# Performance work log

Hardware: AMD Instinct MI355X
Metric: run time of the kernel (lower is better)

The kernel has to match this reference:

```python
import jax, jax.numpy as jnp
import numpy as np

K = 3   # up_kernel
S = 2   # scale_factor per stage
COMP = 64  # compressed channels (mmcv CARAFEPack default)


def _conv2d(x, w, b, pad):
    y = jax.lax.conv_general_dilated(
        x, w, window_strides=(1, 1), padding=[(pad, pad), (pad, pad)],
        dimension_numbers=('NCHW', 'OIHW', 'NCHW'))
    return y + b[None, :, None, None]


def _carafe_stage(x, wc, bc, we, be):
    B, C, H, W = x.shape
    # kernel prediction branch
    comp = _conv2d(x, wc, bc, 0)                 # [B, 64, H, W]
    m = _conv2d(comp, we, be, 1)                 # [B, K*K*S*S, H, W]
    # pixel shuffle: [B, K*K, S, S, H, W] -> [B, K*K, H, S, W, S]
    m = m.reshape(B, K * K, S, S, H, W).transpose(0, 1, 4, 2, 5, 3)
    # softmax over the K*K kernel weights per output pixel
    m = jax.nn.softmax(m, axis=1)                # [B, 9, H, S, W, S]
    # 3x3 neighborhoods of source (row-major kernel order, matching mmcv)
    xp = jnp.pad(x, ((0, 0), (0, 0), (1, 1), (1, 1)))
    patches = jnp.stack(
        [xp[:, :, dy:dy + H, dx:dx + W] for dy in range(K) for dx in range(K)],
        axis=2)                                   # [B, C, 9, H, W]
    # content-aware reassembly: weights shared across channels (up_group=1)
    out = jnp.einsum('bckhw,bkhpwq->bchpwq', patches, m)
    return out.reshape(B, C, S * H, S * W)


def setup_inputs() -> dict:
    key = jax.random.key(0)
    ks = jax.random.split(key, 12)
    B, C, H, W = 2, 256, 16, 16
    inp = {
        'source': jax.random.normal(ks[0], (B, C, H, W), jnp.float32),
        'guidance': jax.random.normal(ks[1], (B, 3, 256, 256), jnp.float32),
    }
    sc = 1.0 / np.sqrt(C)        # fan-in of 1x1 compressor
    se = 1.0 / np.sqrt(COMP * K * K)  # fan-in of 3x3 encoder
    for i in range(4):
        inp[f'wc{i+1}'] = jax.random.normal(ks[2 + 2 * i], (COMP, C, 1, 1), jnp.float32) * sc
        inp[f'bc{i+1}'] = jnp.zeros((COMP,), jnp.float32)
        inp[f'we{i+1}'] = jax.random.normal(ks[3 + 2 * i], (K * K * S * S, COMP, K, K), jnp.float32) * se
        inp[f'be{i+1}'] = jnp.zeros((K * K * S * S,), jnp.float32)
    return inp


def reference(source, guidance,
              wc1, bc1, we1, be1,
              wc2, bc2, we2, be2,
              wc3, bc3, we3, be3,
              wc4, bc4, we4, be4):
    x = _carafe_stage(source, wc1, bc1, we1, be1)
    x = _carafe_stage(x, wc2, bc2, we2, be2)
    x = _carafe_stage(x, wc3, bc3, we3, be3)
    x = _carafe_stage(x, wc4, bc4, we4, be4)
    return x
```

## Files before the change

kernel.cpp:

```cpp
#include <hip/hip_runtime.h>

#define LB __launch_bounds__(256)

__global__ LB void prep_weights(
    const float* __restrict__ wcA, const float* __restrict__ wcB,
    const float* __restrict__ wcC, const float* __restrict__ wcD,
    const float* __restrict__ weA, const float* __restrict__ weB,
    const float* __restrict__ weC, const float* __restrict__ weD,
    float* __restrict__ wcT, float* __restrict__ weT, float* __restrict__ weT3)
{
    int seg = blockIdx.y;
    int t = blockIdx.x * 256 + threadIdx.x;
    if (seg < 4) {
        if (t >= 64 * 256) return;
        const float* w = (seg == 0) ? wcA : (seg == 1) ? wcB : (seg == 2) ? wcC : wcD;
        int c = t & 255, o = t >> 8;
        wcT[seg * 16384 + c * 64 + o] = w[t];
    } else if (seg < 8) {
        if (t >= 36 * 64 * 9) return;
        const float* w = (seg == 4) ? weA : (seg == 5) ? weB : (seg == 6) ? weC : weD;
        int kt = t % 9;
        int r = t / 9;
        int i = r & 63;
        int o = r >> 6;
        int kk = o >> 2, pq = o & 3;
        weT[(seg - 4) * 36864 + ((pq * 64 + i) * 9 + kt) * 16 + kk] = w[t];
    } else {
        if (t >= 36 * 64 * 9) return;
        const float* w = (seg == 8) ? weA : (seg == 9) ? weB : (seg == 10) ? weC : weD;
        int kt = t % 9;
        int r = t / 9;
        int i = r & 63;
        int o = r >> 6;
        weT3[(seg - 8) * 23040 + (i * 9 + kt) * 40 + o] = w[t];
    }
}

template<int OPT>
__global__ LB void compress_flat_k(const float* __restrict__ x, const float* __restrict__ wcO,
                                   const float* __restrict__ bc, float* __restrict__ comp,
                                   int lgW, int lgNpix)
{
    const int lgHW = 2 * lgW;
    const int HW = 1 << lgHW;
    int tid = blockIdx.x * 256 + threadIdx.x;
    int px = tid & ((1 << lgNpix) - 1);
    int og = __builtin_amdgcn_readfirstlane(tid >> lgNpix);
    int b = px >> lgHW;
    int hw = px & (HW - 1);
    const float* xp = x + (((size_t)b * 256) << lgHW) + hw;

    float acc[OPT];
    #pragma unroll
    for (int j = 0; j < OPT; j++) acc[j] = bc[og * OPT + j];

    for (int c0 = 0; c0 < 256; c0 += 8) {
        float xv[8];
        #pragma unroll
        for (int u = 0; u < 8; u++) xv[u] = xp[(size_t)(c0 + u) << lgHW];
        #pragma unroll
        for (int j = 0; j < OPT; j++) {
            const float* wr = wcO + (og * OPT + j) * 256 + c0;
            #pragma unroll
            for (int u = 0; u < 8; u++) acc[j] += wr[u] * xv[u];
        }
    }
    float* op = comp + (((size_t)b * 64 + og * OPT) << lgHW) + hw;
    #pragma unroll
    for (int j = 0; j < OPT; j++) op[(size_t)j << lgHW] = acc[j];
}

__global__ LB void compress_k(const float* __restrict__ x, const float* __restrict__ wcT,
                              const float* __restrict__ bc, float* __restrict__ comp, int lgW)
{
    const int lgHW = 2 * lgW;
    const int HW = 1 << lgHW;
    int lane = threadIdx.x & 63;
    int og = __builtin_amdgcn_readfirstlane(threadIdx.x >> 6);
    int pix = blockIdx.x * 64 + lane;
    int b = pix >> lgHW;
    int hw = pix & (HW - 1);
    const float* xp = x + (((size_t)b * 256) << lgHW) + hw;
    const float* wr = wcT + og * 16;

    float acc[16];
    #pragma unroll
    for (int j = 0; j < 16; j++) acc[j] = bc[og * 16 + j];

    for (int c0 = 0; c0 < 256; c0 += 16) {
        float xv[16];
        #pragma unroll
        for (int u = 0; u < 16; u++)
            xv[u] = xp[(size_t)(c0 + u) << lgHW];
        #pragma unroll
        for (int u = 0; u < 16; u++) {
            const float* w = wr + (c0 + u) * 64;
            float4 w0 = *(const float4*)(w);
            float4 w1 = *(const float4*)(w + 4);
            float4 w2 = *(const float4*)(w + 8);
            float4 w3 = *(const float4*)(w + 12);
            float xu = xv[u];
            acc[0]  += w0.x * xu; acc[1]  += w0.y * xu; acc[2]  += w0.z * xu; acc[3]  += w0.w * xu;
            acc[4]  += w1.x * xu; acc[5]  += w1.y * xu; acc[6]  += w1.z * xu; acc[7]  += w1.w * xu;
            acc[8]  += w2.x * xu; acc[9]  += w2.y * xu; acc[10] += w2.z * xu; acc[11] += w2.w * xu;
            acc[12] += w3.x * xu; acc[13] += w3.y * xu; acc[14] += w3.z * xu; acc[15] += w3.w * xu;
        }
    }

    float* op = comp + (((size_t)b * 64 + og * 16) << lgHW) + hw;
    #pragma unroll
    for (int j = 0; j < 16; j++) op[(size_t)j << lgHW] = acc[j];
}

__global__ LB void encoder_wave_k(const float* __restrict__ comp, const float* __restrict__ weT3,
                                  const float* __restrict__ be, float* __restrict__ mnorm, int lgW)
{
    const int lgHW = 2 * lgW;
    const int HW = 1 << lgHW, W = 1 << lgW, H = W;
    int lane = threadIdx.x & 63;
    int wid = threadIdx.x >> 6;
    int pix = blockIdx.x * 4 + wid;
    int b = pix >> lgHW;
    int hw = pix & (HW - 1);
    int h = hw >> lgW, w = hw & (W - 1);
    int o = lane < 36 ? lane : 35;

    int off[9];
    float msk[9];
    #pragma unroll
    for (int ky = 0; ky < 3; ky++) {
        int ys = h + ky - 1;
        bool yok = (unsigned)ys < (unsigned)H;
        #pragma unroll
        for (int kx = 0; kx < 3; kx++) {
            int xs = w + kx - 1;
            bool ok = yok && ((unsigned)xs < (unsigned)W);
            int kt = ky * 3 + kx;
            off[kt] = ok ? ((ys << lgW) + xs) : 0;
            msk[kt] = ok ? 1.f : 0.f;
        }
    }

    float acc = be[o];
    const float* cb = comp + (((size_t)b) << lgHW) * 64;
    for (int c = 0; c < 64; c += 2) {
        const float* ci0 = cb + ((size_t)c << lgHW);
        const float* ci1 = cb + ((size_t)(c + 1) << lgHW);
        float tap[2][9];
        #pragma unroll
        for (int kt = 0; kt < 9; kt++) tap[0][kt] = ci0[off[kt]];
        #pragma unroll
        for (int kt = 0; kt < 9; kt++) tap[1][kt] = ci1[off[kt]];
        const float* wr0 = weT3 + (c * 9) * 40 + o;
        #pragma unroll
        for (int u = 0; u < 2; u++) {
            #pragma unroll
            for (int kt = 0; kt < 9; kt++)
                acc += wr0[(u * 9 + kt) * 40] * (tap[u][kt] * msk[kt]);
        }
    }

    int pq = o & 3;
    float m = acc;
    #pragma unroll
    for (int j = 0; j < 9; j++) m = fmaxf(m, __shfl(acc, pq + j * 4, 64));
    float e = __expf(acc - m);
    float ssum = 0.f;
    #pragma unroll
    for (int j = 0; j < 9; j++) ssum += __shfl(e, pq + j * 4, 64);
    if (lane < 36)
        mnorm[((((size_t)b * 36) + o) << lgHW) + hw] = e / ssum;
}

__global__ LB void encoder_k(const float* __restrict__ comp, const float* __restrict__ weT,
                             const float* __restrict__ be, float* __restrict__ mnorm, int lgW)
{
    const int lgHW = 2 * lgW;
    const int HW = 1 << lgHW, W = 1 << lgW, H = W;
    int lane = threadIdx.x & 63;
    int pq = __builtin_amdgcn_readfirstlane(threadIdx.x >> 6);
    int pix = blockIdx.x * 64 + lane;
    int b = pix >> lgHW;
    int hw = pix & (HW - 1);
    int h = hw >> lgW, w = hw & (W - 1);

    int off[9];
    float msk[9];
    #pragma unroll
    for (int ky = 0; ky < 3; ky++) {
        int ys = h + ky - 1;
        bool yok = (unsigned)ys < (unsigned)H;
        #pragma unroll
        for (int kx = 0; kx < 3; kx++) {
            int xs = w + kx - 1;
            bool ok = yok && ((unsigned)xs < (unsigned)W);
            int kt = ky * 3 + kx;
            off[kt] = ok ? ((ys << lgW) + xs) : 0;
            msk[kt] = ok ? 1.f : 0.f;
        }
    }

    float acc[9];
    #pragma unroll
    for (int kk = 0; kk < 9; kk++) acc[kk] = be[kk * 4 + pq];

    const float* wp = weT + pq * 9216;
    const float* cb = comp + (((size_t)b) << lgHW) * 64;
    for (int i = 0; i < 64; i += 2) {
        const float* ci0 = cb + ((size_t)i << lgHW);
        const float* ci1 = cb + ((size_t)(i + 1) << lgHW);
        float tap[2][9];
        #pragma unroll
        for (int kt = 0; kt < 9; kt++) tap[0][kt] = ci0[off[kt]];
        #pragma unroll
        for (int kt = 0; kt < 9; kt++) tap[1][kt] = ci1[off[kt]];
        #pragma unroll
        for (int u = 0; u < 2; u++) {
            const float* wi = wp + (i + u) * 144;
            #pragma unroll
            for (int kt = 0; kt < 9; kt++) {
                const float* wt = wi + kt * 16;
                float4 w0 = *(const float4*)(wt);
                float4 w1 = *(const float4*)(wt + 4);
                float  w8 = wt[8];
                float tv = tap[u][kt] * msk[kt];
                acc[0] += w0.x * tv; acc[1] += w0.y * tv; acc[2] += w0.z * tv;
                acc[3] += w0.w * tv; acc[4] += w1.x * tv; acc[5] += w1.y * tv;
                acc[6] += w1.z * tv; acc[7] += w1.w * tv; acc[8] += w8 * tv;
            }
        }
    }

    float m = acc[0];
    #pragma unroll
    for (int kk = 1; kk < 9; kk++) m = fmaxf(m, acc[kk]);
    float s = 0.f;
    #pragma unroll
    for (int kk = 0; kk < 9; kk++) { acc[kk] = __expf(acc[kk] - m); s += acc[kk]; }
    float r = 1.f / s;
    float* mp = mnorm + (((size_t)b * 36) << lgHW) + hw;
    #pragma unroll
    for (int kk = 0; kk < 9; kk++) mp[(size_t)(kk * 4 + pq) << lgHW] = acc[kk] * r;
}

template<int CPT>
__global__ LB void reassembly_k(const float* __restrict__ x, const float* __restrict__ mnorm,
                                float* __restrict__ out, int lgW)
{
    const int lgHW = 2 * lgW;
    const int HW = 1 << lgHW, W = 1 << lgW, H = W;
    int lane = threadIdx.x & 63;
    int cg = threadIdx.x >> 6;
    int nbsh = lgHW - 5;
    int pb = blockIdx.x & ((1 << nbsh) - 1);
    int cs = blockIdx.x >> nbsh;
    int pix = pb * 64 + lane;
    int b = pix >> lgHW;
    int hw = pix & (HW - 1);
    int h = hw >> lgW, w = hw & (W - 1);

    int off[9];
    float msk[9];
    #pragma unroll
    for (int ky = 0; ky < 3; ky++) {
        int ys = h + ky - 1;
        bool yok = (unsigned)ys < (unsigned)H;
        #pragma unroll
        for (int kx = 0; kx < 3; kx++) {
            int xs = w + kx - 1;
            bool ok = yok && ((unsigned)xs < (unsigned)W);
            int kt = ky * 3 + kx;
            off[kt] = ok ? ((ys << lgW) + xs) : 0;
            msk[kt] = ok ? 1.f : 0.f;
        }
    }
    const float* mp = mnorm + (((size_t)b * 36) << lgHW) + hw;
    float wreg[36];
    #pragma unroll
    for (int ch = 0; ch < 36; ch++) wreg[ch] = mp[(size_t)ch << lgHW];

    int c0 = (cs * 4 + cg) * CPT;
    const float* xb = x + ((size_t)b * 256 + c0) * HW;
    size_t OW = (size_t)W * 2;
    float* ob = out + (((size_t)b * 256 + c0) * 2 * H + 2 * h) * OW + 2 * w;
    for (int it = 0; it < CPT; it += 2) {
        const float* xc0 = xb + ((size_t)it << lgHW);
        const float* xc1 = xb + ((size_t)(it + 1) << lgHW);
        float tap[2][9];
        #pragma unroll
        for (int kt = 0; kt < 9; kt++) tap[0][kt] = xc0[off[kt]];
        #pragma unroll
        for (int kt = 0; kt < 9; kt++) tap[1][kt] = xc1[off[kt]];
        #pragma unroll
        for (int u = 0; u < 2; u++) {
            float a00 = 0.f, a01 = 0.f, a10 = 0.f, a11 = 0.f;
            #pragma unroll
            for (int kt = 0; kt < 9; kt++) {
                float tv = tap[u][kt] * msk[kt];
                a00 += tv * wreg[kt * 4 + 0];
                a01 += tv * wreg[kt * 4 + 1];
                a10 += tv * wreg[kt * 4 + 2];
                a11 += tv * wreg[kt * 4 + 3];
            }
            float* oc = ob + (size_t)(it + u) * 2 * H * OW;
            *(float2*)oc = make_float2(a00, a01);
            *(float2*)(oc + OW) = make_float2(a10, a11);
        }
    }
}

extern "C" void kernel_launch(void* const* d_in, const int* in_sizes, int n_in,
                              void* d_out, int out_size, void* d_ws, size_t ws_size,
                              hipStream_t stream)
{
    const float* src = (const float*)d_in[0];
    const float* wc[4]; const float* bc[4]; const float* we[4]; const float* be[4];
    for (int s = 0; s < 4; s++) {
        wc[s] = (const float*)d_in[2 + 4 * s];
        bc[s] = (const float*)d_in[3 + 4 * s];
        we[s] = (const float*)d_in[4 + 4 * s];
        be[s] = (const float*)d_in[5 + 4 * s];
    }
    float* ws   = (float*)d_ws;
    float* x1   = ws;
    float* x2   = x1 + 524288;
    float* x3   = x2 + 2097152;
    float* comp = x3 + 8388608;
    float* mn   = comp + 2097152;
    float* wcT  = mn + 1179648;
    float* weT  = wcT + 65536;
    float* weT3 = weT + 147456;

    prep_weights<<<dim3(81, 12), 256, 0, stream>>>(
        wc[0], wc[1], wc[2], wc[3], we[0], we[1], we[2], we[3], wcT, weT, weT3);

    const float* xin = src;
    float* stage_out[4] = {x1, x2, x3, (float*)d_out};
    int lgW = 4;
    for (int s = 0; s < 4; s++) {
        int lgHW = 2 * lgW;
        int npix = 2 << lgHW;
        int nb = npix >> 6;
        int lgNpix = lgHW + 1;
        if (s < 2)
            compress_flat_k<1><<<npix * 64 / 256, 256, 0, stream>>>(
                xin, wc[s], bc[s], comp, lgW, lgNpix);
        else if (s == 2)
            compress_flat_k<4><<<npix * 16 / 256, 256, 0, stream>>>(
                xin, wc[s], bc[s], comp, lgW, lgNpix);
        else
            compress_k<<<nb, 256, 0, stream>>>(xin, wcT + 3 * 16384, bc[3], comp, lgW);
        if (s < 3)
            encoder_wave_k<<<npix / 4, 256, 0, stream>>>(
                comp, weT3 + s * 23040, be[s], mn, lgW);
        else
            encoder_k<<<nb, 256, 0, stream>>>(comp, weT + 3 * 36864, be[3], mn, lgW);
        if (s < 2)
            reassembly_k<8><<<nb * 8, 256, 0, stream>>>(xin, mn, stage_out[s], lgW);
        else
            reassembly_k<16><<<nb * 4, 256, 0, stream>>>(xin, mn, stage_out[s], lgW);
        xin = stage_out[s];
        lgW++;
    }
}
```

Baseline: 502.6 us.

## Stage final compress and encoder weights in LDS, retune reassembly channel tiling

The final-stage compressor and encoder kernels now load their per-block weight slice into shared memory once, instead of each wave reading weights from global memory. A block now covers 256 pixels and blockIdx.y selects the output group. The weight prep layouts are reorganized to match, with a 12-wide padding for the encoder slices. Reassembly channel-per-thread counts are also retuned per stage (4/8/16/32). This trades extra LDS use and a sync per block for fewer global and L2 weight fetches.

After: 442.8 us. 1.14x faster.

```diff
diff --git a/kernel.cpp b/kernel.cpp
--- a/kernel.cpp
+++ b/kernel.cpp
@@ -7,7 +7,7 @@
     const float* __restrict__ wcC, const float* __restrict__ wcD,
     const float* __restrict__ weA, const float* __restrict__ weB,
     const float* __restrict__ weC, const float* __restrict__ weD,
-    float* __restrict__ wcT, float* __restrict__ weT, float* __restrict__ weT3)
+    float* __restrict__ wcT4, float* __restrict__ weT3, float* __restrict__ weT4)
 {
     int seg = blockIdx.y;
     int t = blockIdx.x * 256 + threadIdx.x;
@@ -15,7 +15,7 @@
         if (t >= 64 * 256) return;
         const float* w = (seg == 0) ? wcA : (seg == 1) ? wcB : (seg == 2) ? wcC : wcD;
         int c = t & 255, o = t >> 8;
-        wcT[seg * 16384 + c * 64 + o] = w[t];
+        wcT4[seg * 16384 + (o >> 4) * 4096 + c * 16 + (o & 15)] = w[t];
     } else if (seg < 8) {
         if (t >= 36 * 64 * 9) return;
         const float* w = (seg == 4) ? weA : (seg == 5) ? weB : (seg == 6) ? weC : weD;
@@ -23,8 +23,7 @@
         int r = t / 9;
         int i = r & 63;
         int o = r >> 6;
-        int kk = o >> 2, pq = o & 3;
-        weT[(seg - 4) * 36864 + ((pq * 64 + i) * 9 + kt) * 16 + kk] = w[t];
+        weT3[(seg - 4) * 23040 + (i * 9 + kt) * 40 + o] = w[t];
     } else {
         if (t >= 36 * 64 * 9) return;
         const float* w = (seg == 8) ? weA : (seg == 9) ? weB : (seg == 10) ? weC : weD;
@@ -32,7 +31,8 @@
         int r = t / 9;
         int i = r & 63;
         int o = r >> 6;
-        weT3[(seg - 8) * 23040 + (i * 9 + kt) * 40 + o] = w[t];
+        int kk = o >> 2, pq = o & 3;
+        weT4[(seg - 8) * 27648 + pq * 6912 + (i * 9 + kt) * 12 + kk] = w[t];
     }
 }
 
@@ -70,31 +70,34 @@
     for (int j = 0; j < OPT; j++) op[(size_t)j << lgHW] = acc[j];
 }
 
-__global__ LB void compress_k(const float* __restrict__ x, const float* __restrict__ wcT,
-                              const float* __restrict__ bc, float* __restrict__ comp, int lgW)
-{
+__global__ LB void compress_lds_k(const float* __restrict__ x, const float* __restrict__ wcT4,
+                                  const float* __restrict__ bc, float* __restrict__ comp, int lgW)
+{
+    __shared__ float wlds[4096];
     const int lgHW = 2 * lgW;
     const int HW = 1 << lgHW;
-    int lane = threadIdx.x & 63;
-    int og = __builtin_amdgcn_readfirstlane(threadIdx.x >> 6);
-    int pix = blockIdx.x * 64 + lane;
-    int b = pix >> lgHW;
-    int hw = pix & (HW - 1);
+    int og = blockIdx.y;
+    for (int t = threadIdx.x; t < 4096; t += 256)
+        wlds[t] = wcT4[og * 4096 + t];
+    __syncthreads();
+
+    int px = blockIdx.x * 256 + threadIdx.x;
+    int b = px >> lgHW;
+    int hw = px & (HW - 1);
     const float* xp = x + (((size_t)b * 256) << lgHW) + hw;
-    const float* wr = wcT + og * 16;
 
     float acc[16];
     #pragma unroll
     for (int j = 0; j < 16; j++) acc[j] = bc[og * 16 + j];
 
-    for (int c0 = 0; c0 < 256; c0 += 16) {
-        float xv[16];
-        #pragma unroll
-        for (int u = 0; u < 16; u++)
+    for (int c0 = 0; c0 < 256; c0 += 8) {
+        float xv[8];
+        #pragma unroll
+        for (int u = 0; u < 8; u++)
             xv[u] = xp[(size_t)(c0 + u) << lgHW];
         #pragma unroll
-        for (int u = 0; u < 16; u++) {
-            const float* w = wr + (c0 + u) * 64;
+        for (int u = 0; u < 8; u++) {
+            const float* w = wlds + (c0 + u) * 16;
             float4 w0 = *(const float4*)(w);
             float4 w1 = *(const float4*)(w + 4);
             float4 w2 = *(const float4*)(w + 8);
@@ -106,7 +109,6 @@
             acc[12] += w3.x * xu; acc[13] += w3.y * xu; acc[14] += w3.z * xu; acc[15] += w3.w * xu;
         }
     }
-
     float* op = comp + (((size_t)b * 64 + og * 16) << lgHW) + hw;
     #pragma unroll
     for (int j = 0; j < 16; j++) op[(size_t)j << lgHW] = acc[j];
@@ -172,16 +174,20 @@
         mnorm[((((size_t)b * 36) + o) << lgHW) + hw] = e / ssum;
 }
 
-__global__ LB void encoder_k(const float* __restrict__ comp, const float* __restrict__ weT,
-                             const float* __restrict__ be, float* __restrict__ mnorm, int lgW)
-{
+__global__ LB void encoder_lds_k(const float* __restrict__ comp, const float* __restrict__ weT4,
+                                 const float* __restrict__ be, float* __restrict__ mnorm, int lgW)
+{
+    __shared__ float wlds[6912];
     const int lgHW = 2 * lgW;
     const int HW = 1 << lgHW, W = 1 << lgW, H = W;
-    int lane = threadIdx.x & 63;
-    int pq = __builtin_amdgcn_readfirstlane(threadIdx.x >> 6);
-    int pix = blockIdx.x * 64 + lane;
-    int b = pix >> lgHW;
-    int hw = pix & (HW - 1);
+    int pq = blockIdx.y;
+    for (int t = threadIdx.x; t < 6912; t += 256)
+        wlds[t] = weT4[pq * 6912 + t];
+    __syncthreads();
+
+    int px = blockIdx.x * 256 + threadIdx.x;
+    int b = px >> lgHW;
+    int hw = px & (HW - 1);
     int h = hw >> lgW, w = hw & (W - 1);
 
     int off[9];
@@ -204,7 +210,6 @@
     #pragma unroll
     for (int kk = 0; kk < 9; kk++) acc[kk] = be[kk * 4 + pq];
 
-    const float* wp = weT + pq * 9216;
     const float* cb = comp + (((size_t)b) << lgHW) * 64;
     for (int i = 0; i < 64; i += 2) {
         const float* ci0 = cb + ((size_t)i << lgHW);
@@ -216,10 +221,10 @@
         for (int kt = 0; kt < 9; kt++) tap[1][kt] = ci1[off[kt]];
         #pragma unroll
         for (int u = 0; u < 2; u++) {
-            const float* wi = wp + (i + u) * 144;
+            const float* wi = wlds + (i + u) * 108;
             #pragma unroll
             for (int kt = 0; kt < 9; kt++) {
-                const float* wt = wi + kt * 16;
+                const float* wt = wi + kt * 12;
                 float4 w0 = *(const float4*)(wt);
                 float4 w1 = *(const float4*)(wt + 4);
                 float  w8 = wt[8];
@@ -327,12 +332,12 @@
     float* x3   = x2 + 2097152;
     float* comp = x3 + 8388608;
     float* mn   = comp + 2097152;
-    float* wcT  = mn + 1179648;
-    float* weT  = wcT + 65536;
-    float* weT3 = weT + 147456;
+    float* wcT4 = mn + 1179648;
+    float* weT3 = wcT4 + 65536;
+    float* weT4 = weT3 + 92160;
 
     prep_weights<<<dim3(81, 12), 256, 0, stream>>>(
-        wc[0], wc[1], wc[2], wc[3], we[0], we[1], we[2], we[3], wcT, weT, weT3);
+        wc[0], wc[1], wc[2], wc[3], we[0], we[1], we[2], we[3], wcT4, weT3, weT4);
 
     const float* xin = src;
     float* stage_out[4] = {x1, x2, x3, (float*)d_out};
@@ -349,16 +354,22 @@
             compress_flat_k<4><<<npix * 16 / 256, 256, 0, stream>>>(
                 xin, wc[s], bc[s], comp, lgW, lgNpix);
         else
-            compress_k<<<nb, 256, 0, stream>>>(xin, wcT + 3 * 16384, bc[3], comp, lgW);
+            compress_lds_k<<<dim3(npix / 256, 4), 256, 0, stream>>>(
+                xin, wcT4 + 3 * 16384, bc[3], comp, lgW);
         if (s < 3)
             encoder_wave_k<<<npix / 4, 256, 0, stream>>>(
                 comp, weT3 + s * 23040, be[s], mn, lgW);
         else
-            encoder_k<<<nb, 256, 0, stream>>>(comp, weT + 3 * 36864, be[3], mn, lgW);
-        if (s < 2)
+            encoder_lds_k<<<dim3(npix / 256, 4), 256, 0, stream>>>(
+                comp, weT4 + 3 * 27648, be[3], mn, lgW);
+        if (s == 0)
+            reassembly_k<4><<<nb * 16, 256, 0, stream>>>(xin, mn, stage_out[s], lgW);
+        else if (s == 1)
             reassembly_k<8><<<nb * 8, 256, 0, stream>>>(xin, mn, stage_out[s], lgW);
+        else if (s == 2)
+            reassembly_k<16><<<nb * 4, 256, 0, stream>>>(xin, mn, stage_out[s], lgW);
         else
-            reassembly_k<16><<<nb * 4, 256, 0, stream>>>(xin, mn, stage_out[s], lgW);
+            reassembly_k<32><<<nb * 2, 256, 0, stream>>>(xin, mn, stage_out[s], lgW);
         xin = stage_out[s];
         lgW++;
     }
```
